# Optimization experiments

Measured on AMD Instinct MI355X. Metric: run time of the kernel, lower is better.

Reference implementation:

```python
import jax, jax.numpy as jnp
import numpy as np

N_NODES = 100000
N_EDGES = 1600000
IN_DIM = 16
HID = 128
N_LAYERS = 3
LN_EPS = 1e-5


def setup_inputs() -> dict:
    key = jax.random.key(0)
    ks = jax.random.split(key, 8)
    x = jax.random.normal(ks[0], (N_NODES, IN_DIM), dtype=jnp.float32)
    edge_index = jax.random.randint(ks[1], (2, N_EDGES), 0, N_NODES, dtype=jnp.int64)
    # input projection params
    W_in = jax.random.normal(ks[2], (IN_DIM, HID), dtype=jnp.float32) * (1.0 / np.sqrt(IN_DIM))
    b_in = jnp.zeros((HID,), dtype=jnp.float32)
    # stacked GCNConv weights [L, H, H] and biases [L, H]
    W_conv = jax.random.normal(ks[3], (N_LAYERS, HID, HID), dtype=jnp.float32) * (1.0 / np.sqrt(HID))
    b_conv = jnp.zeros((N_LAYERS, HID), dtype=jnp.float32)
    # LayerNorm params [L, H]
    ln_gamma = jnp.ones((N_LAYERS, HID), dtype=jnp.float32)
    ln_beta = jnp.zeros((N_LAYERS, HID), dtype=jnp.float32)
    return {"x": x, "edge_index": edge_index, "W_in": W_in, "b_in": b_in,
            "W_conv": W_conv, "b_conv": b_conv, "ln_gamma": ln_gamma, "ln_beta": ln_beta}


def _layer_norm(h, gamma, beta):
    mu = jnp.mean(h, axis=-1, keepdims=True)
    var = jnp.mean(jnp.square(h - mu), axis=-1, keepdims=True)
    return (h - mu) * jax.lax.rsqrt(var + LN_EPS) * gamma + beta


def reference(x, edge_index, W_in, b_in, W_conv, b_conv, ln_gamma, ln_beta):
    N = x.shape[0]
    loops = jnp.arange(N, dtype=edge_index.dtype)
    src = jnp.concatenate([edge_index[0], loops])  # add self-loops (GCNConv default)
    dst = jnp.concatenate([edge_index[1], loops])
    # symmetric normalization D^-1/2 (A+I) D^-1/2
    deg = jax.ops.segment_sum(jnp.ones(src.shape[0], dtype=x.dtype), dst, num_segments=N)
    dis = jax.lax.rsqrt(jnp.maximum(deg, 1.0))  # deg >= 1 with self-loops
    coef = (dis[src] * dis[dst])[:, None]  # [E+N, 1]
    h = x @ W_in + b_in  # input projection -> [N, HID]
    for l in range(N_LAYERS):
        h_prev = h
        m = h @ W_conv[l]  # transform then propagate (same math as GCNConv)
        agg = jax.ops.segment_sum(m[src] * coef, dst, num_segments=N) + b_conv[l]
        h = jax.nn.relu(_layer_norm(agg, ln_gamma[l], ln_beta[l]))
        if l > 0:  # residual only for i > 0, dims always match
            h = h + h_prev
    return h
```

## Files before the change

kernel.cpp:

```cpp
#include <hip/hip_runtime.h>
#include <hip/hip_bf16.h>
#include <hip/hip_fp16.h>

#define HID 128
#define BCHUNK 4096

typedef __attribute__((ext_vector_type(8))) short short8;
typedef __attribute__((ext_vector_type(4))) float f32x4;

__device__ __forceinline__ float ldf(const void* p, size_t i, int bf16f) {
    if (bf16f) {
        unsigned short u = ((const unsigned short*)p)[i];
        union { unsigned int x; float f; } v; v.x = ((unsigned int)u) << 16;
        return v.f;
    }
    return ((const float*)p)[i];
}
__device__ __forceinline__ int ld_idx(const void* p, size_t i, int i64f) {
    return i64f ? (int)((const long long*)p)[i] : ((const int*)p)[i];
}
__device__ __forceinline__ unsigned short f2bfu(float f) {
    __hip_bfloat16 h = __float2bfloat16(f);
    return *reinterpret_cast<unsigned short*>(&h);
}
__device__ __forceinline__ float bflo(unsigned int u) {
    union { unsigned int x; float f; } v; v.x = u << 16;
    return v.f;
}
__device__ __forceinline__ float bfhi(unsigned int u) {
    union { unsigned int x; float f; } v; v.x = u & 0xffff0000u;
    return v.f;
}

__global__ void k_init(const void* __restrict__ gamma, const void* __restrict__ ei,
                       int* flags, int* bkcur, int nbk) {
    int t = threadIdx.x;
    for (int i = t; i < nbk; i += 256) bkcur[i] = 0;
    if (t == 0) {
        unsigned int g0 = ((const unsigned int*)gamma)[0];
        flags[0] = (g0 != 0x3F800000u) ? 1 : 0;
        const unsigned int* e32 = (const unsigned int*)ei;
        int i64 = 1;
        for (int k = 0; k < 128; k++)
            if (e32[2 * k + 1] != 0u) { i64 = 0; break; }
        flags[1] = i64;
    }
}

__global__ __launch_bounds__(256) void k_bucket(const void* __restrict__ ei,
                                                int E, int N, int nbk, int cap,
                                                int* bkcur, unsigned* __restrict__ bdata,
                                                const int* __restrict__ flags) {
    __shared__ int hist[512], base[512];
    int i64 = flags[1];
    int t = threadIdx.x;
    for (int i = t; i < nbk; i += 256) hist[i] = 0;
    __syncthreads();
    int e0 = blockIdx.x * BCHUNK;
    int ss[16], dd[16];
#pragma unroll
    for (int k = 0; k < 16; k++) {
        int e = e0 + k * 256 + t;
        dd[k] = -1;
        if (e < E) {
            int d = ld_idx(ei, (size_t)E + e, i64);
            int s = ld_idx(ei, e, i64);
            if ((unsigned)d < (unsigned)N && (unsigned)s < (unsigned)N) {
                dd[k] = d; ss[k] = s;
                atomicAdd(&hist[d >> 9], 1);
            }
        }
    }
    __syncthreads();
    for (int i = t; i < nbk; i += 256) {
        int c = hist[i];
        base[i] = c ? atomicAdd(&bkcur[i], c) : 0;
        hist[i] = 0;
    }
    __syncthreads();
#pragma unroll
    for (int k = 0; k < 16; k++) {
        if (dd[k] >= 0) {
            int b = dd[k] >> 9;
            int pos = base[b] + atomicAdd(&hist[b], 1);
            if (pos < cap)
                bdata[(size_t)b * cap + pos] =
                    (unsigned)ss[k] | ((unsigned)(dd[k] & 511) << 17);
        }
    }
}

__global__ __launch_bounds__(256) void k_bfused(const int* __restrict__ bkcur,
                                                const unsigned* __restrict__ bdata,
                                                int cap, int* __restrict__ row_ptr,
                                                float* __restrict__ dis,
                                                int* __restrict__ csr_src,
                                                int N, int nbk) {
    __shared__ int hist[512];
    __shared__ int sb[256];
    __shared__ int lsum, bkbase;
    int b = blockIdx.x, t = threadIdx.x;
    int bv = (t < nbk) ? min(bkcur[t], cap) : 0;
    sb[t] = bv;
    __syncthreads();
    int acc = bv;
    for (int off = 1; off < 256; off <<= 1) {
        int x = (t >= off) ? sb[t - off] : 0;
        __syncthreads();
        acc += x; sb[t] = acc;
        __syncthreads();
    }
    if (t == b) bkbase = acc - bv;
    if (b == nbk - 1 && t == nbk - 1) row_ptr[N] = acc;
    for (int i = t; i < 512; i += 256) hist[i] = 0;
    __syncthreads();
    int cb = min(bkcur[b], cap);
    for (int k = t; k < cb; k += 256)
        atomicAdd(&hist[bdata[(size_t)b * cap + k] >> 17], 1);
    __syncthreads();
    int v0 = hist[t], v1 = hist[256 + t];
    int s0 = v0, s1 = v1;
    for (int off = 1; off < 256; off <<= 1) {
        int x0 = (t >= off) ? hist[t - off] : 0;
        int x1 = (t >= off) ? hist[256 + t - off] : 0;
        __syncthreads();
        s0 += x0; s1 += x1;
        hist[t] = s0; hist[256 + t] = s1;
        __syncthreads();
    }
    if (t == 255) lsum = s0;
    __syncthreads();
    int nbase = b << 9;
    int e0 = bkbase + s0 - v0;
    int e1 = bkbase + lsum + s1 - v1;
    if (nbase + t < N) {
        row_ptr[nbase + t] = e0;
        dis[nbase + t] = rsqrtf((float)(v0 + 1));
    }
    if (nbase + 256 + t < N) {
        row_ptr[nbase + 256 + t] = e1;
        dis[nbase + 256 + t] = rsqrtf((float)(v1 + 1));
    }
    __syncthreads();
    hist[t] = e0; hist[256 + t] = e1;
    __syncthreads();
    for (int k = t; k < cb; k += 256) {
        unsigned u = bdata[(size_t)b * cap + k];
        int j = atomicAdd(&hist[u >> 17], 1);
        csr_src[j] = (int)(u & 0x1FFFFu);
    }
}

__global__ __launch_bounds__(256) void k_proj(const void* __restrict__ x,
                       const void* __restrict__ Win, const void* __restrict__ bin,
                       unsigned int* __restrict__ hb2, int N, int mblk,
                       const void* __restrict__ Wc, unsigned short* __restrict__ Wt,
                       const int* __restrict__ flags) {
    int bf = flags[0];
    int t = threadIdx.x;
    if (blockIdx.x >= mblk) {
        int i = (blockIdx.x - mblk) * 256 + t;
        int l = i >> 14, r = i & 16383;
        int n = r >> 7, k = r & 127;
        float w = ldf(Wc, (size_t)l * 16384 + (size_t)k * 128 + n, bf);
        Wt[(size_t)l * 16384 + (size_t)n * 128 + k] = f2bfu(w);
        return;
    }
    int wave = t >> 6, lane = t & 63;
    int wid = blockIdx.x * 4 + wave;
    int nwaves = mblk * 4;
    float w0[16], w1[16];
#pragma unroll
    for (int k = 0; k < 16; k++) {
        w0[k] = ldf(Win, (size_t)k * HID + 2 * lane, bf);
        w1[k] = ldf(Win, (size_t)k * HID + 2 * lane + 1, bf);
    }
    float b0 = ldf(bin, 2 * lane, bf), b1 = ldf(bin, 2 * lane + 1, bf);
    for (int node = wid; node < N; node += nwaves) {
        int nu = __builtin_amdgcn_readfirstlane(node);
        float a0 = b0, a1 = b1;
#pragma unroll
        for (int k = 0; k < 16; k++) {
            float xv = ldf(x, (size_t)nu * 16 + k, bf);
            a0 += xv * w0[k];
            a1 += xv * w1[k];
        }
        hb2[(unsigned)(nu * 64) + lane] =
            (unsigned)f2bfu(a0) | ((unsigned)f2bfu(a1) << 16);
    }
}

__global__ __launch_bounds__(256) void k_gemm(const unsigned short* __restrict__ hb,
                                              const unsigned short* __restrict__ Wt,
                                              const float* __restrict__ dis,
                                              unsigned short* __restrict__ m, int N,
                                              int ntiles) {
    int t = threadIdx.x;
    int wave = t >> 6, lane = t & 63;
    int quad = lane >> 4, n15 = lane & 15;
    short8 bfr[4][8];
#pragma unroll
    for (int kc = 0; kc < 4; kc++)
#pragma unroll
        for (int nt = 0; nt < 8; nt++)
            bfr[kc][nt] = *(const short8*)(Wt + (size_t)(nt * 16 + n15) * HID +
                                           kc * 32 + quad * 8);
    int wid = blockIdx.x * 4 + wave;
    int nwaves = gridDim.x * 4;
    int tile = wid;
    if (tile >= ntiles) return;
    int node = tile * 16 + n15;
    int arow = min(node, N - 1);
    const short8* ap = (const short8*)(hb + (size_t)arow * HID + quad * 8);
    short8 a0 = ap[0], a1 = ap[4], a2 = ap[8], a3 = ap[12];
    float dn = dis[arow];
    while (true) {
        int tile2 = tile + nwaves;
        short8 c0, c1, c2, c3;
        float dn2 = 0.f;
        if (tile2 < ntiles) {
            int ar2 = min(tile2 * 16 + n15, N - 1);
            const short8* ap2 = (const short8*)(hb + (size_t)ar2 * HID + quad * 8);
            c0 = ap2[0]; c1 = ap2[4]; c2 = ap2[8]; c3 = ap2[12];
            dn2 = dis[ar2];
        }
        f32x4 acc[8] = {};
#pragma unroll
        for (int nt = 0; nt < 8; nt++) {
            acc[nt] = __builtin_amdgcn_mfma_f32_16x16x32_bf16(bfr[0][nt], a0, acc[nt], 0, 0, 0);
            acc[nt] = __builtin_amdgcn_mfma_f32_16x16x32_bf16(bfr[1][nt], a1, acc[nt], 0, 0, 0);
            acc[nt] = __builtin_amdgcn_mfma_f32_16x16x32_bf16(bfr[2][nt], a2, acc[nt], 0, 0, 0);
            acc[nt] = __builtin_amdgcn_mfma_f32_16x16x32_bf16(bfr[3][nt], a3, acc[nt], 0, 0, 0);
        }
        if (node < N) {
            unsigned short* mp = m + (size_t)node * HID + quad * 4;
#pragma unroll
            for (int nt = 0; nt < 8; nt++) {
                unsigned lo = (unsigned)f2bfu(acc[nt][0] * dn) |
                              ((unsigned)f2bfu(acc[nt][1] * dn) << 16);
                unsigned hi = (unsigned)f2bfu(acc[nt][2] * dn) |
                              ((unsigned)f2bfu(acc[nt][3] * dn) << 16);
                *(uint2*)(mp + nt * 16) = make_uint2(lo, hi);
            }
        }
        if (tile2 >= ntiles) break;
        a0 = c0; a1 = c1; a2 = c2; a3 = c3; dn = dn2;
        tile = tile2;
        node = tile * 16 + n15;
    }
}

__global__ __launch_bounds__(256) void k_layer(
        const int* __restrict__ row_ptr, const int* __restrict__ csr_src,
        const unsigned int* __restrict__ m2, const float* __restrict__ dis,
        const void* __restrict__ bc, size_t boff,
        const void* __restrict__ lg, const void* __restrict__ lb, size_t goff,
        unsigned int* __restrict__ hb, void* __restrict__ out, int N,
        int res, int last, const int* __restrict__ flags) {
    int t = threadIdx.x, wave = t >> 6, lane = t & 63;
    int wid = blockIdx.x * 4 + wave;
    int nwaves = gridDim.x * 4;
    int bf = flags[0];
    float bb0 = ldf(bc, boff + 2 * lane, bf), bb1 = ldf(bc, boff + 2 * lane + 1, bf);
    float g0 = ldf(lg, goff + 2 * lane, bf), g1 = ldf(lg, goff + 2 * lane + 1, bf);
    float be0 = ldf(lb, goff + 2 * lane, bf), be1 = ldf(lb, goff + 2 * lane + 1, bf);
    unsigned lim = (unsigned)(N - 1);

    for (int node = wid; node < N; node += nwaves) {
        int nodeu = __builtin_amdgcn_readfirstlane(node);
        float dn = dis[nodeu];
        unsigned int ms = m2[(unsigned)(nodeu * 64) + lane];
        float v0 = bflo(ms), v1 = bfhi(ms);
        int begu = __builtin_amdgcn_readfirstlane(row_ptr[nodeu]);
        int endu = __builtin_amdgcn_readfirstlane(row_ptr[nodeu + 1]);
        float p0 = 0.f, p1 = 0.f, q0 = 0.f, q1 = 0.f, r0 = 0.f, r1 = 0.f;
        int j = begu;
        int c0 = 0, c1 = 0, c2 = 0, c3 = 0, c4 = 0, c5 = 0, c6 = 0, c7 = 0;
        if (j + 7 < endu) {
            c0 = csr_src[j];     c1 = csr_src[j + 1];
            c2 = csr_src[j + 2]; c3 = csr_src[j + 3];
            c4 = csr_src[j + 4]; c5 = csr_src[j + 5];
            c6 = csr_src[j + 6]; c7 = csr_src[j + 7];
        }
        while (j + 7 < endu) {
            unsigned int u0 = m2[(unsigned)(c0 * 64) + lane];
            unsigned int u1 = m2[(unsigned)(c1 * 64) + lane];
            unsigned int u2 = m2[(unsigned)(c2 * 64) + lane];
            unsigned int u3 = m2[(unsigned)(c3 * 64) + lane];
            unsigned int u4 = m2[(unsigned)(c4 * 64) + lane];
            unsigned int u5 = m2[(unsigned)(c5 * 64) + lane];
            unsigned int u6 = m2[(unsigned)(c6 * 64) + lane];
            unsigned int u7 = m2[(unsigned)(c7 * 64) + lane];
            int jn = j + 8;
            int pj = min(jn, max(endu - 8, begu));
            int n0 = csr_src[pj],     n1 = csr_src[pj + 1];
            int n2 = csr_src[pj + 2], n3 = csr_src[pj + 3];
            int n4 = csr_src[pj + 4], n5 = csr_src[pj + 5];
            int n6 = csr_src[pj + 6], n7 = csr_src[pj + 7];
            v0 += bflo(u0); v1 += bfhi(u0);
            p0 += bflo(u1); p1 += bfhi(u1);
            q0 += bflo(u2); q1 += bfhi(u2);
            r0 += bflo(u3); r1 += bfhi(u3);
            v0 += bflo(u4); v1 += bfhi(u4);
            p0 += bflo(u5); p1 += bfhi(u5);
            q0 += bflo(u6); q1 += bfhi(u6);
            r0 += bflo(u7); r1 += bfhi(u7);
            c0 = n0; c1 = n1; c2 = n2; c3 = n3;
            c4 = n4; c5 = n5; c6 = n6; c7 = n7;
            j = jn;
        }
        if (j < endu) {
            int s0 = (int)min((unsigned)csr_src[j], lim);
            int s1 = (j + 1 < endu) ? (int)min((unsigned)csr_src[j + 1], lim) : s0;
            int s2 = (j + 2 < endu) ? (int)min((unsigned)csr_src[j + 2], lim) : s0;
            int s3 = (j + 3 < endu) ? (int)min((unsigned)csr_src[j + 3], lim) : s0;
            int s4 = (j + 4 < endu) ? (int)min((unsigned)csr_src[j + 4], lim) : s0;
            int s5 = (j + 5 < endu) ? (int)min((unsigned)csr_src[j + 5], lim) : s0;
            int s6 = (j + 6 < endu) ? (int)min((unsigned)csr_src[j + 6], lim) : s0;
            int s7 = (j + 7 < endu) ? (int)min((unsigned)csr_src[j + 7], lim) : s0;
            unsigned int u0 = m2[(unsigned)(s0 * 64) + lane];
            unsigned int u1 = m2[(unsigned)(s1 * 64) + lane];
            unsigned int u2 = m2[(unsigned)(s2 * 64) + lane];
            unsigned int u3 = m2[(unsigned)(s3 * 64) + lane];
            unsigned int u4 = m2[(unsigned)(s4 * 64) + lane];
            unsigned int u5 = m2[(unsigned)(s5 * 64) + lane];
            unsigned int u6 = m2[(unsigned)(s6 * 64) + lane];
            unsigned int u7 = m2[(unsigned)(s7 * 64) + lane];
            u1 = (j + 1 < endu) ? u1 : 0u;
            u2 = (j + 2 < endu) ? u2 : 0u;
            u3 = (j + 3 < endu) ? u3 : 0u;
            u4 = (j + 4 < endu) ? u4 : 0u;
            u5 = (j + 5 < endu) ? u5 : 0u;
            u6 = (j + 6 < endu) ? u6 : 0u;
            u7 = (j + 7 < endu) ? u7 : 0u;
            v0 += bflo(u0); v1 += bfhi(u0);
            p0 += bflo(u1); p1 += bfhi(u1);
            q0 += bflo(u2); q1 += bfhi(u2);
            r0 += bflo(u3); r1 += bfhi(u3);
            v0 += bflo(u4); v1 += bfhi(u4);
            p0 += bflo(u5); p1 += bfhi(u5);
            q0 += bflo(u6); q1 += bfhi(u6);
            r0 += bflo(u7); r1 += bfhi(u7);
        }
        v0 += p0 + q0 + r0;
        v1 += p1 + q1 + r1;
        v0 = bb0 + v0 * dn;
        v1 = bb1 + v1 * dn;
        float s1 = v0 + v1, s2 = v0 * v0 + v1 * v1;
#pragma unroll
        for (int o = 32; o; o >>= 1) {
            s1 += __shfl_down(s1, o);
            s2 += __shfl_down(s2, o);
        }
        float sum = __shfl(s1, 0), sq = __shfl(s2, 0);
        float mu = sum * (1.0f / HID);
        float var = sq * (1.0f / HID) - mu * mu;
        float r = rsqrtf(var + 1e-5f);
        float o0 = fmaxf((v0 - mu) * r * g0 + be0, 0.f);
        float o1 = fmaxf((v1 - mu) * r * g1 + be1, 0.f);
        size_t widx = (size_t)nodeu * 64 + lane;
        if (res) {
            unsigned int hp = hb[widx];
            o0 += bflo(hp);
            o1 += bfhi(hp);
        }
        unsigned int packed = (unsigned int)f2bfu(o0) | ((unsigned int)f2bfu(o1) << 16);
        hb[widx] = packed;
        if (last) {
            if (bf) ((unsigned int*)out)[widx] = packed;
            else {
                size_t base = (size_t)nodeu * HID + 2 * lane;
                *(float2*)&((float*)out)[base] = make_float2(o0, o1);
            }
        }
    }
}

extern "C" void kernel_launch(void* const* d_in, const int* in_sizes, int n_in,
                              void* d_out, int out_size, void* d_ws, size_t ws_size,
                              hipStream_t stream) {
    const void* x   = d_in[0];
    const void* ei  = d_in[1];
    const void* Win = d_in[2];
    const void* bin = d_in[3];
    const void* Wc  = d_in[4];
    const void* bc  = d_in[5];
    const void* lg  = d_in[6];
    const void* lb  = d_in[7];

    int N = in_sizes[0] / 16;
    int E = in_sizes[1] / 2;
    int nbk = (N + 511) >> 9;
    int cap = ((E / nbk) * 2 + 255) & ~255;

    char* ws = (char*)d_ws;
    size_t off = 0;
    auto alloc = [&](size_t bytes) {
        void* p = ws + off;
        off += (bytes + 255) / 256 * 256;
        return p;
    };
    int*            flags    = (int*)alloc(256);
    float*          dis      = (float*)alloc((size_t)N * 4);
    int*            row_ptr  = (int*)alloc(((size_t)N + 1) * 4);
    int*            bkcur    = (int*)alloc((size_t)nbk * 4);
    unsigned*       bdata    = (unsigned*)alloc((size_t)nbk * cap * 4);
    int*            csr_src  = (int*)alloc((size_t)E * 4 + 64);
    unsigned short* hb       = (unsigned short*)alloc((size_t)N * HID * 2);
    unsigned short* m        = (unsigned short*)alloc((size_t)N * HID * 2);
    unsigned short* Wt       = (unsigned short*)alloc((size_t)3 * HID * HID * 2);
    (void)ws_size;

    k_init<<<1, 256, 0, stream>>>(lg, ei, flags, bkcur, nbk);
    k_bucket<<<(E + BCHUNK - 1) / BCHUNK, 256, 0, stream>>>(ei, E, N, nbk, cap,
                                                            bkcur, bdata, flags);
    k_bfused<<<nbk, 256, 0, stream>>>(bkcur, bdata, cap, row_ptr, dis, csr_src,
                                      N, nbk);
    int mblk = 2048;
    k_proj<<<mblk + 192, 256, 0, stream>>>(x, Win, bin, (unsigned int*)hb, N, mblk,
                                           Wc, Wt, flags);

    int ntiles = (N + 15) / 16;
    int lblocks = min((N + 3) / 4, 2048);
    for (int l = 0; l < 3; l++) {
        k_gemm<<<512, 256, 0, stream>>>(hb, Wt + (size_t)l * HID * HID, dis, m, N,
                                        ntiles);
        k_layer<<<lblocks, 256, 0, stream>>>(row_ptr, csr_src,
                                             (const unsigned int*)m, dis, bc,
                                             (size_t)l * HID, lg, lb, (size_t)l * HID,
                                             (unsigned int*)hb, d_out, N,
                                             l > 0, l == 2, flags);
    }
}
```

Measured before the change: 415.0 us.

## Slice feature matrix into column chunks for cache-local gather, split LayerNorm

The GEMM now writes the transformed features in a sliced layout: 8 slices of 16 columns, each slice contiguous across nodes. A new gather kernel assigns each block to one slice, so the random neighbour reads stay within a smaller region that fits in cache better. Each wave handles 8 edges at once with 8 lanes per edge. The aggregated result goes to a bf16 scratch buffer that reuses the bucket storage, and a separate LayerNorm kernel then reads it. In exchange there is an extra kernel launch, an extra round trip of the aggregate through memory, bf16 rounding of the aggregate, and 32-byte-granular gathers.

```diff
diff --git a/kernel.cpp b/kernel.cpp
--- a/kernel.cpp
+++ b/kernel.cpp
@@ -193,7 +193,7 @@
 __global__ __launch_bounds__(256) void k_gemm(const unsigned short* __restrict__ hb,
                                               const unsigned short* __restrict__ Wt,
                                               const float* __restrict__ dis,
-                                              unsigned short* __restrict__ m, int N,
+                                              unsigned int* __restrict__ mfs, int N,
                                               int ntiles) {
     int t = threadIdx.x;
     int wave = t >> 6, lane = t & 63;
@@ -233,14 +233,14 @@
             acc[nt] = __builtin_amdgcn_mfma_f32_16x16x32_bf16(bfr[3][nt], a3, acc[nt], 0, 0, 0);
         }
         if (node < N) {
-            unsigned short* mp = m + (size_t)node * HID + quad * 4;
 #pragma unroll
             for (int nt = 0; nt < 8; nt++) {
                 unsigned lo = (unsigned)f2bfu(acc[nt][0] * dn) |
                               ((unsigned)f2bfu(acc[nt][1] * dn) << 16);
                 unsigned hi = (unsigned)f2bfu(acc[nt][2] * dn) |
                               ((unsigned)f2bfu(acc[nt][3] * dn) << 16);
-                *(uint2*)(mp + nt * 16) = make_uint2(lo, hi);
+                *(uint2*)(mfs + ((size_t)nt * N + node) * 8 + quad * 2) =
+                    make_uint2(lo, hi);
             }
         }
         if (tile2 >= ntiles) break;
@@ -250,10 +250,40 @@
     }
 }
 
-__global__ __launch_bounds__(256) void k_layer(
-        const int* __restrict__ row_ptr, const int* __restrict__ csr_src,
-        const unsigned int* __restrict__ m2, const float* __restrict__ dis,
-        const void* __restrict__ bc, size_t boff,
+__global__ __launch_bounds__(256) void k_gath(const int* __restrict__ row_ptr,
+        const int* __restrict__ csr_src, const unsigned* __restrict__ mfs,
+        unsigned* __restrict__ agg, int N) {
+    int t = threadIdx.x, wave = t >> 6, lane = t & 63;
+    int s = blockIdx.x & 7;
+    int wis = (blockIdx.x >> 3) * 4 + wave;
+    int nws = (gridDim.x >> 3) * 4;
+    const unsigned* base = mfs + (size_t)s * N * 8;
+    int esub = lane >> 3, d = lane & 7;
+    for (int node = wis; node < N; node += nws) {
+        int nodeu = __builtin_amdgcn_readfirstlane(node);
+        int begu = __builtin_amdgcn_readfirstlane(row_ptr[nodeu]);
+        int endu = __builtin_amdgcn_readfirstlane(row_ptr[nodeu + 1]);
+        float a0 = 0.f, a1 = 0.f;
+        for (int j = begu; j < endu; j += 8) {
+            int e = j + esub;
+            int idx = csr_src[min(e, endu - 1)];
+            unsigned u = base[(unsigned)(idx * 8) + d];
+            if (e < endu) { a0 += bflo(u); a1 += bfhi(u); }
+        }
+        a0 += __shfl_xor(a0, 8);  a1 += __shfl_xor(a1, 8);
+        a0 += __shfl_xor(a0, 16); a1 += __shfl_xor(a1, 16);
+        a0 += __shfl_xor(a0, 32); a1 += __shfl_xor(a1, 32);
+        if (lane < 8) {
+            unsigned su = base[(unsigned)(nodeu * 8) + d];
+            a0 += bflo(su); a1 += bfhi(su);
+            agg[(unsigned)(nodeu * 64) + s * 8 + d] =
+                (unsigned)f2bfu(a0) | ((unsigned)f2bfu(a1) << 16);
+        }
+    }
+}
+
+__global__ __launch_bounds__(256) void k_ln(const unsigned* __restrict__ agg,
+        const float* __restrict__ dis, const void* __restrict__ bc, size_t boff,
         const void* __restrict__ lg, const void* __restrict__ lb, size_t goff,
         unsigned int* __restrict__ hb, void* __restrict__ out, int N,
         int res, int last, const int* __restrict__ flags) {
@@ -264,88 +294,12 @@
     float bb0 = ldf(bc, boff + 2 * lane, bf), bb1 = ldf(bc, boff + 2 * lane + 1, bf);
     float g0 = ldf(lg, goff + 2 * lane, bf), g1 = ldf(lg, goff + 2 * lane + 1, bf);
     float be0 = ldf(lb, goff + 2 * lane, bf), be1 = ldf(lb, goff + 2 * lane + 1, bf);
-    unsigned lim = (unsigned)(N - 1);
-
     for (int node = wid; node < N; node += nwaves) {
         int nodeu = __builtin_amdgcn_readfirstlane(node);
         float dn = dis[nodeu];
-        unsigned int ms = m2[(unsigned)(nodeu * 64) + lane];
-        float v0 = bflo(ms), v1 = bfhi(ms);
-        int begu = __builtin_amdgcn_readfirstlane(row_ptr[nodeu]);
-        int endu = __builtin_amdgcn_readfirstlane(row_ptr[nodeu + 1]);
-        float p0 = 0.f, p1 = 0.f, q0 = 0.f, q1 = 0.f, r0 = 0.f, r1 = 0.f;
-        int j = begu;
-        int c0 = 0, c1 = 0, c2 = 0, c3 = 0, c4 = 0, c5 = 0, c6 = 0, c7 = 0;
-        if (j + 7 < endu) {
-            c0 = csr_src[j];     c1 = csr_src[j + 1];
-            c2 = csr_src[j + 2]; c3 = csr_src[j + 3];
-            c4 = csr_src[j + 4]; c5 = csr_src[j + 5];
-            c6 = csr_src[j + 6]; c7 = csr_src[j + 7];
-        }
-        while (j + 7 < endu) {
-            unsigned int u0 = m2[(unsigned)(c0 * 64) + lane];
-            unsigned int u1 = m2[(unsigned)(c1 * 64) + lane];
-            unsigned int u2 = m2[(unsigned)(c2 * 64) + lane];
-            unsigned int u3 = m2[(unsigned)(c3 * 64) + lane];
-            unsigned int u4 = m2[(unsigned)(c4 * 64) + lane];
-            unsigned int u5 = m2[(unsigned)(c5 * 64) + lane];
-            unsigned int u6 = m2[(unsigned)(c6 * 64) + lane];
-            unsigned int u7 = m2[(unsigned)(c7 * 64) + lane];
-            int jn = j + 8;
-            int pj = min(jn, max(endu - 8, begu));
-            int n0 = csr_src[pj],     n1 = csr_src[pj + 1];
-            int n2 = csr_src[pj + 2], n3 = csr_src[pj + 3];
-            int n4 = csr_src[pj + 4], n5 = csr_src[pj + 5];
-            int n6 = csr_src[pj + 6], n7 = csr_src[pj + 7];
-            v0 += bflo(u0); v1 += bfhi(u0);
-            p0 += bflo(u1); p1 += bfhi(u1);
-            q0 += bflo(u2); q1 += bfhi(u2);
-            r0 += bflo(u3); r1 += bfhi(u3);
-            v0 += bflo(u4); v1 += bfhi(u4);
-            p0 += bflo(u5); p1 += bfhi(u5);
-            q0 += bflo(u6); q1 += bfhi(u6);
-            r0 += bflo(u7); r1 += bfhi(u7);
-            c0 = n0; c1 = n1; c2 = n2; c3 = n3;
-            c4 = n4; c5 = n5; c6 = n6; c7 = n7;
-            j = jn;
-        }
-        if (j < endu) {
-            int s0 = (int)min((unsigned)csr_src[j], lim);
-            int s1 = (j + 1 < endu) ? (int)min((unsigned)csr_src[j + 1], lim) : s0;
-            int s2 = (j + 2 < endu) ? (int)min((unsigned)csr_src[j + 2], lim) : s0;
-            int s3 = (j + 3 < endu) ? (int)min((unsigned)csr_src[j + 3], lim) : s0;
-            int s4 = (j + 4 < endu) ? (int)min((unsigned)csr_src[j + 4], lim) : s0;
-            int s5 = (j + 5 < endu) ? (int)min((unsigned)csr_src[j + 5], lim) : s0;
-            int s6 = (j + 6 < endu) ? (int)min((unsigned)csr_src[j + 6], lim) : s0;
-            int s7 = (j + 7 < endu) ? (int)min((unsigned)csr_src[j + 7], lim) : s0;
-            unsigned int u0 = m2[(unsigned)(s0 * 64) + lane];
-            unsigned int u1 = m2[(unsigned)(s1 * 64) + lane];
-            unsigned int u2 = m2[(unsigned)(s2 * 64) + lane];
-            unsigned int u3 = m2[(unsigned)(s3 * 64) + lane];
-            unsigned int u4 = m2[(unsigned)(s4 * 64) + lane];
-            unsigned int u5 = m2[(unsigned)(s5 * 64) + lane];
-            unsigned int u6 = m2[(unsigned)(s6 * 64) + lane];
-            unsigned int u7 = m2[(unsigned)(s7 * 64) + lane];
-            u1 = (j + 1 < endu) ? u1 : 0u;
-            u2 = (j + 2 < endu) ? u2 : 0u;
-            u3 = (j + 3 < endu) ? u3 : 0u;
-            u4 = (j + 4 < endu) ? u4 : 0u;
-            u5 = (j + 5 < endu) ? u5 : 0u;
-            u6 = (j + 6 < endu) ? u6 : 0u;
-            u7 = (j + 7 < endu) ? u7 : 0u;
-            v0 += bflo(u0); v1 += bfhi(u0);
-            p0 += bflo(u1); p1 += bfhi(u1);
-            q0 += bflo(u2); q1 += bfhi(u2);
-            r0 += bflo(u3); r1 += bfhi(u3);
-            v0 += bflo(u4); v1 += bfhi(u4);
-            p0 += bflo(u5); p1 += bfhi(u5);
-            q0 += bflo(u6); q1 += bfhi(u6);
-            r0 += bflo(u7); r1 += bfhi(u7);
-        }
-        v0 += p0 + q0 + r0;
-        v1 += p1 + q1 + r1;
-        v0 = bb0 + v0 * dn;
-        v1 = bb1 + v1 * dn;
+        unsigned av = agg[(unsigned)(nodeu * 64) + lane];
+        float v0 = bb0 + bflo(av) * dn;
+        float v1 = bb1 + bfhi(av) * dn;
         float s1 = v0 + v1, s2 = v0 * v0 + v1 * v1;
 #pragma unroll
         for (int o = 32; o; o >>= 1) {
@@ -400,16 +354,21 @@
         off += (bytes + 255) / 256 * 256;
         return p;
     };
+    size_t bdata_bytes = (size_t)nbk * cap * 4;
+    size_t agg_bytes   = (size_t)N * 64 * 4;
     int*            flags    = (int*)alloc(256);
     float*          dis      = (float*)alloc((size_t)N * 4);
     int*            row_ptr  = (int*)alloc(((size_t)N + 1) * 4);
     int*            bkcur    = (int*)alloc((size_t)nbk * 4);
-    unsigned*       bdata    = (unsigned*)alloc((size_t)nbk * cap * 4);
+    unsigned*       scratch  = (unsigned*)alloc(bdata_bytes > agg_bytes ?
+                                                bdata_bytes : agg_bytes);
     int*            csr_src  = (int*)alloc((size_t)E * 4 + 64);
     unsigned short* hb       = (unsigned short*)alloc((size_t)N * HID * 2);
     unsigned short* m        = (unsigned short*)alloc((size_t)N * HID * 2);
     unsigned short* Wt       = (unsigned short*)alloc((size_t)3 * HID * HID * 2);
     (void)ws_size;
+    unsigned* bdata = scratch;
+    unsigned* agg   = scratch;
 
     k_init<<<1, 256, 0, stream>>>(lg, ei, flags, bkcur, nbk);
     k_bucket<<<(E + BCHUNK - 1) / BCHUNK, 256, 0, stream>>>(ei, E, N, nbk, cap,
@@ -421,14 +380,14 @@
                                            Wc, Wt, flags);
 
     int ntiles = (N + 15) / 16;
-    int lblocks = min((N + 3) / 4, 2048);
     for (int l = 0; l < 3; l++) {
-        k_gemm<<<512, 256, 0, stream>>>(hb, Wt + (size_t)l * HID * HID, dis, m, N,
-                                        ntiles);
-        k_layer<<<lblocks, 256, 0, stream>>>(row_ptr, csr_src,
-                                             (const unsigned int*)m, dis, bc,
-                                             (size_t)l * HID, lg, lb, (size_t)l * HID,
-                                             (unsigned int*)hb, d_out, N,
-                                             l > 0, l == 2, flags);
-    }
-}
+        k_gemm<<<512, 256, 0, stream>>>(hb, Wt + (size_t)l * HID * HID, dis,
+                                        (unsigned int*)m, N, ntiles);
+        k_gath<<<2048, 256, 0, stream>>>(row_ptr, csr_src, (const unsigned*)m,
+                                         agg, N);
+        k_ln<<<2048, 256, 0, stream>>>(agg, dis, bc, (size_t)l * HID,
+                                       lg, lb, (size_t)l * HID,
+                                       (unsigned int*)hb, d_out, N,
+                                       l > 0, l == 2, flags);
+    }
+}
```

New measurement: 844.7 us. 2.04x slower.
